# Performance work log

Measured on AMD Instinct MI355X. Metric: run time of the kernel, lower is better.

## Reference

```python
import jax, jax.numpy as jnp
import numpy as np

B, S, D_IN = 1, 2048, 2048
H, KV, HD = 32, 8, 64          # num_heads, num_kv_groups, head_dim
GS = H // KV                    # group_size
D_OUT = H * HD
EPS = 1e-6


def _rmsnorm(x, w):
    # RMSNormQwen over last dim (head_dim)
    var = jnp.mean(x * x, axis=-1, keepdims=True)
    return x * jax.lax.rsqrt(var + EPS) * w


def _rope(x, cos, sin):
    # rotate-half RoPE; x: [B, heads, S, HD], cos/sin: [S, HD]
    d = x.shape[-1]
    x1, x2 = x[..., : d // 2], x[..., d // 2 :]
    rot = jnp.concatenate([-x2, x1], axis=-1)
    return x * cos + rot * sin


def setup_inputs() -> dict:
    key = jax.random.key(0)
    ks = jax.random.split(key, 8)
    x = jax.random.normal(ks[0], (B, S, D_IN), dtype=jnp.float32)
    Wq = jax.random.normal(ks[1], (D_IN, D_OUT), dtype=jnp.float32) * 0.02
    Wk = jax.random.normal(ks[2], (D_IN, KV * HD), dtype=jnp.float32) * 0.02
    Wv = jax.random.normal(ks[3], (D_IN, KV * HD), dtype=jnp.float32) * 0.02
    Wo = jax.random.normal(ks[4], (D_OUT, D_IN), dtype=jnp.float32) * 0.02
    q_norm_w = jnp.ones((HD,), dtype=jnp.float32)
    k_norm_w = jnp.ones((HD,), dtype=jnp.float32)
    # causal mask: True where masked (j > i)
    mask = jnp.triu(jnp.ones((S, S), dtype=bool), k=1)
    # RoPE tables
    inv_freq = 1.0 / (10000.0 ** (np.arange(0, HD, 2, dtype=np.float32) / HD))
    ang = np.arange(S, dtype=np.float32)[:, None] * inv_freq[None, :]  # [S, HD/2]
    cos = jnp.asarray(np.concatenate([np.cos(ang), np.cos(ang)], axis=-1))
    sin = jnp.asarray(np.concatenate([np.sin(ang), np.sin(ang)], axis=-1))
    return {"x": x, "mask": mask, "cos": cos, "sin": sin,
            "Wq": Wq, "Wk": Wk, "Wv": Wv, "Wo": Wo,
            "q_norm_w": q_norm_w, "k_norm_w": k_norm_w}


def reference(x, mask, cos, sin, Wq, Wk, Wv, Wo, q_norm_w, k_norm_w):
    b, s, _ = x.shape
    q = (x @ Wq).reshape(b, s, H, HD).transpose(0, 2, 1, 3)   # [B,H,S,HD]
    k = (x @ Wk).reshape(b, s, KV, HD).transpose(0, 2, 1, 3)  # [B,KV,S,HD]
    v = (x @ Wv).reshape(b, s, KV, HD).transpose(0, 2, 1, 3)  # [B,KV,S,HD]
    q = _rmsnorm(q, q_norm_w)
    k = _rmsnorm(k, k_norm_w)
    q = _rope(q, cos, sin)
    k = _rope(k, cos, sin)
    # grouped-KV attention without materializing repeated K/V
    qg = q.reshape(b, KV, GS, s, HD)
    scores = jnp.einsum('bkgsd,bktd->bkgst', qg, k)           # [B,KV,GS,S,S]
    scores = jnp.where(mask, -jnp.inf, scores)
    weights = jax.nn.softmax(scores / (HD ** 0.5), axis=-1)
    ctx = jnp.einsum('bkgst,bktd->bkgsd', weights, v)         # [B,KV,GS,S,HD]
    ctx = ctx.reshape(b, H, s, HD).transpose(0, 2, 1, 3).reshape(b, s, D_OUT)
    return ctx @ Wo
```

## Files before the change

### kernel.cpp

```cpp
#include <hip/hip_runtime.h>
#include <hip/hip_bf16.h>
#include <math.h>

#define S_LEN 2048
#define DIN   2048
#define NH    32
#define NKV   8
#define HD    64
#define DOUT  2048
#define QKVN  3072
#define KOFF  2048
#define VOFF  2560

typedef __attribute__((ext_vector_type(8))) short short8v;
typedef __attribute__((ext_vector_type(8))) unsigned short ushort8v;
typedef __attribute__((ext_vector_type(4))) float float4v;

__device__ __forceinline__ float bf2f(unsigned short u) {
    union { float f; unsigned u; } c; c.u = ((unsigned)u) << 16; return c.f;
}
__device__ __forceinline__ unsigned short f2bf(float f) {
    union { float f; unsigned u; } c; c.f = f;
    unsigned r = c.u + 0x7fffu + ((c.u >> 16) & 1u);
    return (unsigned short)(r >> 16);
}

__global__ __launch_bounds__(256) void cvt_bf16(const float* __restrict__ in,
                                                unsigned short* __restrict__ out, int n) {
    int i = (blockIdx.x * 256 + threadIdx.x) * 4;
    if (i >= n) return;
    float4 t = *(const float4*)(in + i);
    out[i + 0] = f2bf(t.x); out[i + 1] = f2bf(t.y);
    out[i + 2] = f2bf(t.z); out[i + 3] = f2bf(t.w);
}

__global__ __launch_bounds__(256) void transpose_cvt(const float* __restrict__ in,
                                                     unsigned short* __restrict__ out,
                                                     int K, int N) {
    __shared__ float t[32][33];
    const int k0 = blockIdx.y * 32, n0 = blockIdx.x * 32;
#pragma unroll
    for (int j = threadIdx.y; j < 32; j += 8)
        t[j][threadIdx.x] = in[(size_t)(k0 + j) * N + n0 + threadIdx.x];
    __syncthreads();
#pragma unroll
    for (int j = threadIdx.y; j < 32; j += 8)
        out[(size_t)(n0 + j) * K + k0 + threadIdx.x] = f2bf(t[threadIdx.x][j]);
}

__global__ __launch_bounds__(256) void transpose_qkv(const float* __restrict__ Wq,
                                                     const float* __restrict__ Wk,
                                                     const float* __restrict__ Wv,
                                                     unsigned short* __restrict__ out) {
    __shared__ float t[32][33];
    const int n0 = blockIdx.x * 32, k0 = blockIdx.y * 32;
    const float* src; int nn0, Nsrc;
    if (n0 < KOFF)      { src = Wq; nn0 = n0;        Nsrc = DOUT; }
    else if (n0 < VOFF) { src = Wk; nn0 = n0 - KOFF; Nsrc = 512; }
    else                { src = Wv; nn0 = n0 - VOFF; Nsrc = 512; }
#pragma unroll
    for (int j = threadIdx.y; j < 32; j += 8)
        t[j][threadIdx.x] = src[(size_t)(k0 + j) * Nsrc + nn0 + threadIdx.x];
    __syncthreads();
#pragma unroll
    for (int j = threadIdx.y; j < 32; j += 8)
        out[(size_t)(n0 + j) * DIN + k0 + threadIdx.x] = f2bf(t[threadIdx.x][j]);
}

template <int FUSE>
__global__ __launch_bounds__(256) void gemm64(const unsigned short* __restrict__ A,
                                              const unsigned short* __restrict__ Bt,
                                              void* __restrict__ Cv, int M, int N, int K,
                                              const float* __restrict__ qnw,
                                              const float* __restrict__ knw,
                                              const float* __restrict__ cosb,
                                              const float* __restrict__ sinb) {
    __shared__ __attribute__((aligned(16))) unsigned short As[128 * 32];
    __shared__ __attribute__((aligned(16))) unsigned short Bs[64 * 32];
    const int tid = threadIdx.x, lane = tid & 63, w = tid >> 6;
    const int bm = blockIdx.y * 128, bn = blockIdx.x * 64;
    const int wm = w * 32;

    float4v acc[2][4];
#pragma unroll
    for (int i = 0; i < 2; i++)
#pragma unroll
        for (int j = 0; j < 4; j++) acc[i][j] = (float4v){0.f, 0.f, 0.f, 0.f};

    const int lr = lane >> 2, lc = (lane & 3) * 8;
    const unsigned short* Ag0 = A + (size_t)(bm + w * 32 + lr) * K + lc;
    const unsigned short* Ag1 = Ag0 + (size_t)16 * K;
    const unsigned short* Bg  = Bt + (size_t)(bn + w * 16 + lr) * K + lc;
    unsigned short* Al0 = As + (w * 32) * 32;
    unsigned short* Al1 = As + (w * 32 + 16) * 32;
    unsigned short* Bl  = Bs + (w * 16) * 32;

    const int frow = lane & 15, fk = (lane >> 4) * 8;

    for (int k0 = 0; k0 < K; k0 += 32) {
        __syncthreads();
        __builtin_amdgcn_global_load_lds(
            (const __attribute__((address_space(1))) void*)(Ag0 + k0),
            (__attribute__((address_space(3))) void*)Al0, 16, 0, 0);
        __builtin_amdgcn_global_load_lds(
            (const __attribute__((address_space(1))) void*)(Ag1 + k0),
            (__attribute__((address_space(3))) void*)Al1, 16, 0, 0);
        __builtin_amdgcn_global_load_lds(
            (const __attribute__((address_space(1))) void*)(Bg + k0),
            (__attribute__((address_space(3))) void*)Bl, 16, 0, 0);
        __syncthreads();

        short8v af[2], bf[4];
#pragma unroll
        for (int fm = 0; fm < 2; fm++)
            af[fm] = *(const short8v*)(As + (wm + fm * 16 + frow) * 32 + fk);
#pragma unroll
        for (int fn = 0; fn < 4; fn++)
            bf[fn] = *(const short8v*)(Bs + (fn * 16 + frow) * 32 + fk);
#pragma unroll
        for (int fm = 0; fm < 2; fm++)
#pragma unroll
            for (int fn = 0; fn < 4; fn++)
                acc[fm][fn] = __builtin_amdgcn_mfma_f32_16x16x32_bf16(
                    af[fm], bf[fn], acc[fm][fn], 0, 0, 0);
    }

    const int quad = lane >> 4, col16 = lane & 15;
    if constexpr (FUSE == 1) {
        unsigned short* C = (unsigned short*)Cv;
        const int head = bn >> 6;
        if (head < 40) {
            const float* nw = (head < 32) ? qnw : knw;
            float wv[4];
#pragma unroll
            for (int fn = 0; fn < 4; fn++) wv[fn] = nw[fn * 16 + col16];
#pragma unroll
            for (int fm = 0; fm < 2; fm++)
#pragma unroll
                for (int r = 0; r < 4; r++) {
                    float x0 = acc[fm][0][r], x1 = acc[fm][1][r];
                    float x2 = acc[fm][2][r], x3 = acc[fm][3][r];
                    float ss = x0 * x0 + x1 * x1 + x2 * x2 + x3 * x3;
                    ss += __shfl_xor(ss, 1); ss += __shfl_xor(ss, 2);
                    ss += __shfl_xor(ss, 4); ss += __shfl_xor(ss, 8);
                    const float inv = rsqrtf(ss * (1.0f / 64.0f) + 1e-6f);
                    float xn[4] = {x0 * inv * wv[0], x1 * inv * wv[1],
                                   x2 * inv * wv[2], x3 * inv * wv[3]};
                    const int row = bm + wm + fm * 16 + quad * 4 + r;
                    const float* cr = cosb + (size_t)row * HD;
                    const float* sr = sinb + (size_t)row * HD;
#pragma unroll
                    for (int fn = 0; fn < 4; fn++) {
                        const float rot = (fn < 2) ? -xn[fn + 2] : xn[fn - 2];
                        const float res = xn[fn] * cr[fn * 16 + col16] +
                                          rot * sr[fn * 16 + col16];
                        C[(size_t)row * N + bn + fn * 16 + col16] = f2bf(res);
                    }
                }
        } else {
#pragma unroll
            for (int fm = 0; fm < 2; fm++)
#pragma unroll
                for (int fn = 0; fn < 4; fn++)
#pragma unroll
                    for (int r = 0; r < 4; r++)
                        C[(size_t)(bm + wm + fm * 16 + quad * 4 + r) * N +
                          bn + fn * 16 + col16] = f2bf(acc[fm][fn][r]);
        }
    } else {
        float* C = (float*)Cv;
#pragma unroll
        for (int fm = 0; fm < 2; fm++)
#pragma unroll
            for (int fn = 0; fn < 4; fn++)
#pragma unroll
                for (int r = 0; r < 4; r++)
                    C[(size_t)(bm + wm + fm * 16 + quad * 4 + r) * N +
                      bn + fn * 16 + col16] = acc[fm][fn][r];
    }
}

#define PSTR 88

__global__ __launch_bounds__(256) void flash_mfma(const unsigned short* __restrict__ qb,
                                                  const unsigned short* __restrict__ kb,
                                                  const unsigned short* __restrict__ vb,
                                                  unsigned short* __restrict__ ob) {
    __shared__ __attribute__((aligned(16))) unsigned short Ks[2][64 * PSTR];
    __shared__ __attribute__((aligned(16))) unsigned short Vt[2][64 * PSTR];
    __shared__ __attribute__((aligned(16))) unsigned short Ps[128 * PSTR];

    const int tid = threadIdx.x, lane = tid & 63, w = tid >> 6;
    const int col = lane & 15, quad = lane >> 4;
    const int bid = blockIdx.x;
    const int g = bid & 7;
    const int bx = bid >> 3;
    const int s0 = (63 - bx) * 32;
    const int h = g * 4 + w;

    const float C1 = 0.18033688011112042f;
    const float C2 = 12.262908856239697f;

    short8v qf[2][2];
#pragma unroll
    for (int mf = 0; mf < 2; mf++)
#pragma unroll
        for (int ks = 0; ks < 2; ks++)
            qf[mf][ks] = *(const short8v*)(qb + (size_t)(s0 + mf * 16 + col) * QKVN +
                                           h * HD + ks * 32 + quad * 8);

    float4v O[2][4];
    float lsum[2][4];
#pragma unroll
    for (int mf = 0; mf < 2; mf++) {
#pragma unroll
        for (int df = 0; df < 4; df++) O[mf][df] = (float4v){0.f, 0.f, 0.f, 0.f};
#pragma unroll
        for (int r = 0; r < 4; r++) lsum[mf][r] = 0.f;
    }

    const int kkey = tid >> 2, kch = tid & 3;
    const unsigned short* kg = kb + (size_t)kkey * QKVN + g * HD + kch * 16;
    const int vkey = tid & 63, vdb = tid >> 6;
    const unsigned short* vg = vb + (size_t)vkey * QKVN + g * HD + vdb * 16;

    ushort8v ka0 = *(const ushort8v*)kg;
    ushort8v ka1 = *(const ushort8v*)(kg + 8);
    ushort8v va0 = *(const ushort8v*)vg;
    ushort8v va1 = *(const ushort8v*)(vg + 8);

    const int nt = (s0 + 32 + 63) >> 6;
    for (int it = 0; it < nt; it++) {
        const int c = it & 1;
        {
            unsigned short* kd = Ks[c] + kkey * PSTR + kch * 16;
            *(ushort8v*)kd = ka0;
            *(ushort8v*)(kd + 8) = ka1;
            unsigned short* vd = Vt[c] + (size_t)(vdb * 16) * PSTR + vkey;
#pragma unroll
            for (int j = 0; j < 8; j++) vd[j * PSTR] = va0[j];
#pragma unroll
            for (int j = 0; j < 8; j++) vd[(8 + j) * PSTR] = va1[j];
        }
        __syncthreads();
        if (it + 1 < nt) {
            const size_t off = (size_t)(it + 1) * 64 * QKVN;
            ka0 = *(const ushort8v*)(kg + off);
            ka1 = *(const ushort8v*)(kg + off + 8);
            va0 = *(const ushort8v*)(vg + off);
            va1 = *(const ushort8v*)(vg + off + 8);
        }

        const int t0 = it * 64;
        const bool edge = (t0 + 63 > s0);

        short8v kf[4][2];
#pragma unroll
        for (int nf = 0; nf < 4; nf++)
#pragma unroll
            for (int ks = 0; ks < 2; ks++)
                kf[nf][ks] = *(const short8v*)(Ks[c] + (nf * 16 + col) * PSTR +
                                               ks * 32 + quad * 8);

#pragma unroll
        for (int mf = 0; mf < 2; mf++) {
            float4v sc[4];
#pragma unroll
            for (int nf = 0; nf < 4; nf++) {
                sc[nf] = (float4v){0.f, 0.f, 0.f, 0.f};
#pragma unroll
                for (int ks = 0; ks < 2; ks++)
                    sc[nf] = __builtin_amdgcn_mfma_f32_16x16x32_bf16(qf[mf][ks], kf[nf][ks],
                                                                     sc[nf], 0, 0, 0);
            }
#pragma unroll
            for (int nf = 0; nf < 4; nf++)
#pragma unroll
                for (int r = 0; r < 4; r++) {
                    float arg = sc[nf][r] * C1 - C2;
                    if (edge) {
                        const int qg = s0 + mf * 16 + quad * 4 + r;
                        const int kg_ = t0 + nf * 16 + col;
                        arg = (kg_ <= qg) ? arg : -100.f;
                    }
                    const float p = exp2f(arg);
                    sc[nf][r] = p;
                    lsum[mf][r] += p;
                }
            unsigned short* pw = Ps + (size_t)(w * 32 + mf * 16 + quad * 4) * PSTR;
#pragma unroll
            for (int nf = 0; nf < 4; nf++) {
                const int pb = (nf ^ quad) * 16;
#pragma unroll
                for (int r = 0; r < 4; r++)
                    pw[r * PSTR + pb + col] = f2bf(sc[nf][r]);
            }
        }

        short8v vf[4][2];
#pragma unroll
        for (int df = 0; df < 4; df++)
#pragma unroll
            for (int ks = 0; ks < 2; ks++)
                vf[df][ks] = *(const short8v*)(Vt[c] + (df * 16 + col) * PSTR +
                                               ks * 32 + quad * 8);
#pragma unroll
        for (int mf = 0; mf < 2; mf++)
#pragma unroll
            for (int ks = 0; ks < 2; ks++) {
                const int lb = ks * 2 + (quad >> 1);
                short8v pf = *(const short8v*)(Ps + (size_t)(w * 32 + mf * 16 + col) * PSTR +
                                               ((lb ^ (col >> 2)) * 16 + (quad & 1) * 8));
#pragma unroll
                for (int df = 0; df < 4; df++)
                    O[mf][df] = __builtin_amdgcn_mfma_f32_16x16x32_bf16(pf, vf[df][ks],
                                                                        O[mf][df], 0, 0, 0);
            }
    }

#pragma unroll
    for (int mf = 0; mf < 2; mf++)
#pragma unroll
        for (int r = 0; r < 4; r++) {
            float l = lsum[mf][r];
            l += __shfl_xor(l, 1); l += __shfl_xor(l, 2);
            l += __shfl_xor(l, 4); l += __shfl_xor(l, 8);
            lsum[mf][r] = 1.0f / l;
        }
#pragma unroll
    for (int mf = 0; mf < 2; mf++)
#pragma unroll
        for (int df = 0; df < 4; df++)
#pragma unroll
            for (int r = 0; r < 4; r++) {
                float v = O[mf][df][r] * lsum[mf][r];
                ob[(size_t)(s0 + mf * 16 + quad * 4 + r) * DOUT + h * HD + df * 16 + col] = f2bf(v);
            }
}

extern "C" void kernel_launch(void* const* d_in, const int* in_sizes, int n_in,
                              void* d_out, int out_size, void* d_ws, size_t ws_size,
                              hipStream_t stream) {
    const float* x    = (const float*)d_in[0];
    const float* cosb = (const float*)d_in[2];
    const float* sinb = (const float*)d_in[3];
    const float* Wq   = (const float*)d_in[4];
    const float* Wk   = (const float*)d_in[5];
    const float* Wv   = (const float*)d_in[6];
    const float* Wo   = (const float*)d_in[7];
    const float* qw   = (const float*)d_in[8];
    const float* kw   = (const float*)d_in[9];
    float* out = (float*)d_out;

    unsigned short* W1  = (unsigned short*)d_ws;
    unsigned short* XB  = W1 + (size_t)QKVN * DIN;
    unsigned short* QKV = XB + (size_t)S_LEN * DIN;

    dim3 blk256(256);
    dim3 tblk(32, 8);

    transpose_qkv<<<dim3(QKVN / 32, DIN / 32), tblk, 0, stream>>>(Wq, Wk, Wv, W1);
    cvt_bf16<<<dim3(S_LEN * DIN / 4 / 256), blk256, 0, stream>>>(x, XB, S_LEN * DIN);

    gemm64<1><<<dim3(QKVN / 64, S_LEN / 128), blk256, 0, stream>>>(
        XB, W1, QKV, S_LEN, QKVN, DIN, qw, kw, cosb, sinb);

    flash_mfma<<<dim3((S_LEN / 32) * NKV), blk256, 0, stream>>>(
        QKV, QKV + KOFF, QKV + VOFF, XB);

    transpose_cvt<<<dim3(DIN / 32, DOUT / 32), tblk, 0, stream>>>(Wo, W1, DOUT, DIN);
    gemm64<0><<<dim3(DIN / 64, S_LEN / 128), blk256, 0, stream>>>(
        XB, W1, out, S_LEN, DIN, DOUT, nullptr, nullptr, nullptr, nullptr);
}
```

Baseline: 285.0 us.

## Halve flash query tile, stream K from global into registers, merge prep kernels

The attention kernel now gives each wave 16 query rows instead of 32, doubling the grid. It drops the shared-memory K buffer in favour of per-lane K fragments loaded and prefetched directly from global memory, and shrinks the LDS pad stride. Blocks are ordered in a zig-zag over sequence tiles to balance causal work, with launch bounds requesting higher occupancy. The three weight/input conversion kernels are merged into one prep launch that writes a separate WoT buffer. The trade-off is that K is re-read from global per wave and per group of 16 rows, adding redundant global traffic.

```diff
diff --git a/kernel.cpp b/kernel.cpp
--- a/kernel.cpp
+++ b/kernel.cpp
@@ -25,46 +25,46 @@
     return (unsigned short)(r >> 16);
 }
 
-__global__ __launch_bounds__(256) void cvt_bf16(const float* __restrict__ in,
-                                                unsigned short* __restrict__ out, int n) {
-    int i = (blockIdx.x * 256 + threadIdx.x) * 4;
-    if (i >= n) return;
-    float4 t = *(const float4*)(in + i);
-    out[i + 0] = f2bf(t.x); out[i + 1] = f2bf(t.y);
-    out[i + 2] = f2bf(t.z); out[i + 3] = f2bf(t.w);
-}
-
-__global__ __launch_bounds__(256) void transpose_cvt(const float* __restrict__ in,
-                                                     unsigned short* __restrict__ out,
-                                                     int K, int N) {
+__global__ __launch_bounds__(256) void prep(const float* __restrict__ Wq,
+                                            const float* __restrict__ Wk,
+                                            const float* __restrict__ Wv,
+                                            const float* __restrict__ Wo,
+                                            const float* __restrict__ x,
+                                            unsigned short* __restrict__ W1,
+                                            unsigned short* __restrict__ WoT,
+                                            unsigned short* __restrict__ XB) {
     __shared__ float t[32][33];
-    const int k0 = blockIdx.y * 32, n0 = blockIdx.x * 32;
-#pragma unroll
-    for (int j = threadIdx.y; j < 32; j += 8)
-        t[j][threadIdx.x] = in[(size_t)(k0 + j) * N + n0 + threadIdx.x];
-    __syncthreads();
-#pragma unroll
-    for (int j = threadIdx.y; j < 32; j += 8)
-        out[(size_t)(n0 + j) * K + k0 + threadIdx.x] = f2bf(t[threadIdx.x][j]);
-}
-
-__global__ __launch_bounds__(256) void transpose_qkv(const float* __restrict__ Wq,
-                                                     const float* __restrict__ Wk,
-                                                     const float* __restrict__ Wv,
-                                                     unsigned short* __restrict__ out) {
-    __shared__ float t[32][33];
-    const int n0 = blockIdx.x * 32, k0 = blockIdx.y * 32;
-    const float* src; int nn0, Nsrc;
-    if (n0 < KOFF)      { src = Wq; nn0 = n0;        Nsrc = DOUT; }
-    else if (n0 < VOFF) { src = Wk; nn0 = n0 - KOFF; Nsrc = 512; }
-    else                { src = Wv; nn0 = n0 - VOFF; Nsrc = 512; }
-#pragma unroll
-    for (int j = threadIdx.y; j < 32; j += 8)
-        t[j][threadIdx.x] = src[(size_t)(k0 + j) * Nsrc + nn0 + threadIdx.x];
-    __syncthreads();
-#pragma unroll
-    for (int j = threadIdx.y; j < 32; j += 8)
-        out[(size_t)(n0 + j) * DIN + k0 + threadIdx.x] = f2bf(t[threadIdx.x][j]);
+    const int a = blockIdx.x;
+    const int tx = threadIdx.x & 31, ty = threadIdx.x >> 5;
+    if (a < 6144) {
+        const int n0 = (a % 96) * 32, k0 = (a / 96) * 32;
+        const float* src; int nn0, Nsrc;
+        if (n0 < KOFF)      { src = Wq; nn0 = n0;        Nsrc = DOUT; }
+        else if (n0 < VOFF) { src = Wk; nn0 = n0 - KOFF; Nsrc = 512; }
+        else                { src = Wv; nn0 = n0 - VOFF; Nsrc = 512; }
+#pragma unroll
+        for (int j = ty; j < 32; j += 8)
+            t[j][tx] = src[(size_t)(k0 + j) * Nsrc + nn0 + tx];
+        __syncthreads();
+#pragma unroll
+        for (int j = ty; j < 32; j += 8)
+            W1[(size_t)(n0 + j) * DIN + k0 + tx] = f2bf(t[tx][j]);
+    } else if (a < 10240) {
+        const int b = a - 6144;
+        const int n0 = (b % 64) * 32, k0 = (b / 64) * 32;
+#pragma unroll
+        for (int j = ty; j < 32; j += 8)
+            t[j][tx] = Wo[(size_t)(k0 + j) * DIN + n0 + tx];
+        __syncthreads();
+#pragma unroll
+        for (int j = ty; j < 32; j += 8)
+            WoT[(size_t)(n0 + j) * DOUT + k0 + tx] = f2bf(t[tx][j]);
+    } else {
+        const int i = (a - 10240) * 1024 + threadIdx.x * 4;
+        float4 v = *(const float4*)(x + i);
+        XB[i + 0] = f2bf(v.x); XB[i + 1] = f2bf(v.y);
+        XB[i + 2] = f2bf(v.z); XB[i + 3] = f2bf(v.w);
+    }
 }
 
 template <int FUSE>
@@ -180,62 +180,60 @@
     }
 }
 
-#define PSTR 88
-
-__global__ __launch_bounds__(256) void flash_mfma(const unsigned short* __restrict__ qb,
-                                                  const unsigned short* __restrict__ kb,
-                                                  const unsigned short* __restrict__ vb,
-                                                  unsigned short* __restrict__ ob) {
-    __shared__ __attribute__((aligned(16))) unsigned short Ks[2][64 * PSTR];
+#define PSTR 72
+
+__global__ __launch_bounds__(256, 4) void flash_mfma(const unsigned short* __restrict__ qb,
+                                                     const unsigned short* __restrict__ kb,
+                                                     const unsigned short* __restrict__ vb,
+                                                     unsigned short* __restrict__ ob) {
     __shared__ __attribute__((aligned(16))) unsigned short Vt[2][64 * PSTR];
-    __shared__ __attribute__((aligned(16))) unsigned short Ps[128 * PSTR];
+    __shared__ __attribute__((aligned(16))) unsigned short Ps[64 * PSTR];
 
     const int tid = threadIdx.x, lane = tid & 63, w = tid >> 6;
     const int col = lane & 15, quad = lane >> 4;
     const int bid = blockIdx.x;
     const int g = bid & 7;
     const int bx = bid >> 3;
-    const int s0 = (63 - bx) * 32;
+    const int kk = bx >> 5, bb = bx & 31;
+    const int tile = (kk == 0) ? bb : (kk == 1) ? 63 - bb : (kk == 2) ? 64 + bb : 127 - bb;
+    const int s0 = tile * 16;
     const int h = g * 4 + w;
 
     const float C1 = 0.18033688011112042f;
     const float C2 = 12.262908856239697f;
 
-    short8v qf[2][2];
-#pragma unroll
-    for (int mf = 0; mf < 2; mf++)
-#pragma unroll
-        for (int ks = 0; ks < 2; ks++)
-            qf[mf][ks] = *(const short8v*)(qb + (size_t)(s0 + mf * 16 + col) * QKVN +
-                                           h * HD + ks * 32 + quad * 8);
-
-    float4v O[2][4];
-    float lsum[2][4];
-#pragma unroll
-    for (int mf = 0; mf < 2; mf++) {
-#pragma unroll
-        for (int df = 0; df < 4; df++) O[mf][df] = (float4v){0.f, 0.f, 0.f, 0.f};
-#pragma unroll
-        for (int r = 0; r < 4; r++) lsum[mf][r] = 0.f;
-    }
-
-    const int kkey = tid >> 2, kch = tid & 3;
-    const unsigned short* kg = kb + (size_t)kkey * QKVN + g * HD + kch * 16;
+    short8v qf[2];
+#pragma unroll
+    for (int ks = 0; ks < 2; ks++)
+        qf[ks] = *(const short8v*)(qb + (size_t)(s0 + col) * QKVN +
+                                   h * HD + ks * 32 + quad * 8);
+
+    float4v O[4];
+    float lsum[4];
+#pragma unroll
+    for (int df = 0; df < 4; df++) O[df] = (float4v){0.f, 0.f, 0.f, 0.f};
+#pragma unroll
+    for (int r = 0; r < 4; r++) lsum[r] = 0.f;
+
     const int vkey = tid & 63, vdb = tid >> 6;
     const unsigned short* vg = vb + (size_t)vkey * QKVN + g * HD + vdb * 16;
-
-    ushort8v ka0 = *(const ushort8v*)kg;
-    ushort8v ka1 = *(const ushort8v*)(kg + 8);
     ushort8v va0 = *(const ushort8v*)vg;
     ushort8v va1 = *(const ushort8v*)(vg + 8);
 
-    const int nt = (s0 + 32 + 63) >> 6;
+    const unsigned short* kgb = kb + (size_t)col * QKVN + g * HD + quad * 8;
+
+    short8v kf[4][2];
+#pragma unroll
+    for (int nf = 0; nf < 4; nf++)
+#pragma unroll
+        for (int ks = 0; ks < 2; ks++)
+            kf[nf][ks] = *(const short8v*)(kgb + (size_t)(nf * 16) * QKVN + ks * 32);
+
+    const int nt = (s0 + 79) >> 6;
     for (int it = 0; it < nt; it++) {
         const int c = it & 1;
+        const int t0 = it * 64;
         {
-            unsigned short* kd = Ks[c] + kkey * PSTR + kch * 16;
-            *(ushort8v*)kd = ka0;
-            *(ushort8v*)(kd + 8) = ka1;
             unsigned short* vd = Vt[c] + (size_t)(vdb * 16) * PSTR + vkey;
 #pragma unroll
             for (int j = 0; j < 8; j++) vd[j * PSTR] = va0[j];
@@ -245,49 +243,47 @@
         __syncthreads();
         if (it + 1 < nt) {
             const size_t off = (size_t)(it + 1) * 64 * QKVN;
-            ka0 = *(const ushort8v*)(kg + off);
-            ka1 = *(const ushort8v*)(kg + off + 8);
             va0 = *(const ushort8v*)(vg + off);
             va1 = *(const ushort8v*)(vg + off + 8);
         }
 
-        const int t0 = it * 64;
         const bool edge = (t0 + 63 > s0);
 
-        short8v kf[4][2];
+        float4v sc[4];
+#pragma unroll
+        for (int nf = 0; nf < 4; nf++) {
+            sc[nf] = (float4v){0.f, 0.f, 0.f, 0.f};
+#pragma unroll
+            for (int ks = 0; ks < 2; ks++)
+                sc[nf] = __builtin_amdgcn_mfma_f32_16x16x32_bf16(qf[ks], kf[nf][ks],
+                                                                 sc[nf], 0, 0, 0);
+        }
+        if (it + 1 < nt) {
+            const size_t off = (size_t)(t0 + 64) * QKVN;
+#pragma unroll
+            for (int nf = 0; nf < 4; nf++)
+#pragma unroll
+                for (int ks = 0; ks < 2; ks++)
+                    kf[nf][ks] = *(const short8v*)(kgb + off + (size_t)(nf * 16) * QKVN +
+                                                   ks * 32);
+        }
+
 #pragma unroll
         for (int nf = 0; nf < 4; nf++)
 #pragma unroll
-            for (int ks = 0; ks < 2; ks++)
-                kf[nf][ks] = *(const short8v*)(Ks[c] + (nf * 16 + col) * PSTR +
-                                               ks * 32 + quad * 8);
-
-#pragma unroll
-        for (int mf = 0; mf < 2; mf++) {
-            float4v sc[4];
-#pragma unroll
-            for (int nf = 0; nf < 4; nf++) {
-                sc[nf] = (float4v){0.f, 0.f, 0.f, 0.f};
-#pragma unroll
-                for (int ks = 0; ks < 2; ks++)
-                    sc[nf] = __builtin_amdgcn_mfma_f32_16x16x32_bf16(qf[mf][ks], kf[nf][ks],
-                                                                     sc[nf], 0, 0, 0);
+            for (int r = 0; r < 4; r++) {
+                float arg = sc[nf][r] * C1 - C2;
+                if (edge) {
+                    const int qg = s0 + quad * 4 + r;
+                    const int kg_ = t0 + nf * 16 + col;
+                    arg = (kg_ <= qg) ? arg : -100.f;
+                }
+                const float p = exp2f(arg);
+                sc[nf][r] = p;
+                lsum[r] += p;
             }
-#pragma unroll
-            for (int nf = 0; nf < 4; nf++)
-#pragma unroll
-                for (int r = 0; r < 4; r++) {
-                    float arg = sc[nf][r] * C1 - C2;
-                    if (edge) {
-                        const int qg = s0 + mf * 16 + quad * 4 + r;
-                        const int kg_ = t0 + nf * 16 + col;
-                        arg = (kg_ <= qg) ? arg : -100.f;
-                    }
-                    const float p = exp2f(arg);
-                    sc[nf][r] = p;
-                    lsum[mf][r] += p;
-                }
-            unsigned short* pw = Ps + (size_t)(w * 32 + mf * 16 + quad * 4) * PSTR;
+        {
+            unsigned short* pw = Ps + (size_t)(w * 16 + quad * 4) * PSTR;
 #pragma unroll
             for (int nf = 0; nf < 4; nf++) {
                 const int pb = (nf ^ quad) * 16;
@@ -305,37 +301,31 @@
                 vf[df][ks] = *(const short8v*)(Vt[c] + (df * 16 + col) * PSTR +
                                                ks * 32 + quad * 8);
 #pragma unroll
-        for (int mf = 0; mf < 2; mf++)
-#pragma unroll
-            for (int ks = 0; ks < 2; ks++) {
-                const int lb = ks * 2 + (quad >> 1);
-                short8v pf = *(const short8v*)(Ps + (size_t)(w * 32 + mf * 16 + col) * PSTR +
-                                               ((lb ^ (col >> 2)) * 16 + (quad & 1) * 8));
-#pragma unroll
-                for (int df = 0; df < 4; df++)
-                    O[mf][df] = __builtin_amdgcn_mfma_f32_16x16x32_bf16(pf, vf[df][ks],
-                                                                        O[mf][df], 0, 0, 0);
-            }
-    }
-
-#pragma unroll
-    for (int mf = 0; mf < 2; mf++)
+        for (int ks = 0; ks < 2; ks++) {
+            const int lb = ks * 2 + (quad >> 1);
+            short8v pf = *(const short8v*)(Ps + (size_t)(w * 16 + col) * PSTR +
+                                           ((lb ^ (col >> 2)) * 16 + (quad & 1) * 8));
+#pragma unroll
+            for (int df = 0; df < 4; df++)
+                O[df] = __builtin_amdgcn_mfma_f32_16x16x32_bf16(pf, vf[df][ks],
+                                                                O[df], 0, 0, 0);
+        }
+    }
+
+#pragma unroll
+    for (int r = 0; r < 4; r++) {
+        float l = lsum[r];
+        l += __shfl_xor(l, 1); l += __shfl_xor(l, 2);
+        l += __shfl_xor(l, 4); l += __shfl_xor(l, 8);
+        lsum[r] = 1.0f / l;
+    }
+#pragma unroll
+    for (int df = 0; df < 4; df++)
 #pragma unroll
         for (int r = 0; r < 4; r++) {
-            float l = lsum[mf][r];
-            l += __shfl_xor(l, 1); l += __shfl_xor(l, 2);
-            l += __shfl_xor(l, 4); l += __shfl_xor(l, 8);
-            lsum[mf][r] = 1.0f / l;
-        }
-#pragma unroll
-    for (int mf = 0; mf < 2; mf++)
-#pragma unroll
-        for (int df = 0; df < 4; df++)
-#pragma unroll
-            for (int r = 0; r < 4; r++) {
-                float v = O[mf][df][r] * lsum[mf][r];
-                ob[(size_t)(s0 + mf * 16 + quad * 4 + r) * DOUT + h * HD + df * 16 + col] = f2bf(v);
-            }
+            float v = O[df][r] * lsum[r];
+            ob[(size_t)(s0 + quad * 4 + r) * DOUT + h * HD + df * 16 + col] = f2bf(v);
+        }
 }
 
 extern "C" void kernel_launch(void* const* d_in, const int* in_sizes, int n_in,
@@ -353,22 +343,20 @@
     float* out = (float*)d_out;
 
     unsigned short* W1  = (unsigned short*)d_ws;
-    unsigned short* XB  = W1 + (size_t)QKVN * DIN;
+    unsigned short* WoT = W1 + (size_t)QKVN * DIN;
+    unsigned short* XB  = WoT + (size_t)DIN * DOUT;
     unsigned short* QKV = XB + (size_t)S_LEN * DIN;
 
     dim3 blk256(256);
-    dim3 tblk(32, 8);
-
-    transpose_qkv<<<dim3(QKVN / 32, DIN / 32), tblk, 0, stream>>>(Wq, Wk, Wv, W1);
-    cvt_bf16<<<dim3(S_LEN * DIN / 4 / 256), blk256, 0, stream>>>(x, XB, S_LEN * DIN);
+
+    prep<<<dim3(14336), blk256, 0, stream>>>(Wq, Wk, Wv, Wo, x, W1, WoT, XB);
 
     gemm64<1><<<dim3(QKVN / 64, S_LEN / 128), blk256, 0, stream>>>(
         XB, W1, QKV, S_LEN, QKVN, DIN, qw, kw, cosb, sinb);
 
-    flash_mfma<<<dim3((S_LEN / 32) * NKV), blk256, 0, stream>>>(
+    flash_mfma<<<dim3((S_LEN / 16) * NKV), blk256, 0, stream>>>(
         QKV, QKV + KOFF, QKV + VOFF, XB);
 
-    transpose_cvt<<<dim3(DIN / 32, DOUT / 32), tblk, 0, stream>>>(Wo, W1, DOUT, DIN);
     gemm64<0><<<dim3(DIN / 64, S_LEN / 128), blk256, 0, stream>>>(
-        XB, W1, out, S_LEN, DIN, DOUT, nullptr, nullptr, nullptr, nullptr);
-}
+        XB, WoT, out, S_LEN, DIN, DOUT, nullptr, nullptr, nullptr, nullptr);
+}
```

After: 303.0 us. 6.3% more time.
